# Performance work log

Measured on AMD Instinct MI355X. Metric: run time of the kernel, lower is better.

The kernel has to match this reference:

```python
import jax, jax.numpy as jnp
import numpy as np

K = 3      # kernel_size
PAD = 1    # padding


def _unfold(x, k, pad):
    # torch.nn.functional.unfold, stride=1, dilation=1.
    # Returns (B, C*k*k, L) with channel-major, then kernel-row, kernel-col ordering.
    B, C, H, W = x.shape
    xp = jnp.pad(x, ((0, 0), (0, 0), (pad, pad), (pad, pad)))
    Ho = H + 2 * pad - k + 1
    Wo = W + 2 * pad - k + 1
    cols = jnp.stack([xp[:, :, i:i + Ho, j:j + Wo]
                      for i in range(k) for j in range(k)], axis=2)  # (B,C,k*k,Ho,Wo)
    return cols.reshape(B, C * k * k, Ho * Wo)


def _fold_nonoverlap(pcols, C, k, pad, out_size):
    # torch.nn.functional.fold with kernel_size=k, stride=k (non-overlapping tiles),
    # padding=pad, output_size=(out_size, out_size).
    B = pcols.shape[0]
    bh = (out_size + 2 * pad - k) // k + 1  # blocks per spatial dim
    t = pcols.reshape(B, C, k, k, bh, bh)
    t = t.transpose(0, 1, 4, 2, 5, 3).reshape(B, C, bh * k, bh * k)  # tiled canvas
    # canvas position = tile position - pad; crop window [pad, pad+out_size)
    t = jnp.pad(t, ((0, 0), (0, 0), (0, pad), (0, pad)))
    return t[:, :, pad:pad + out_size, pad:pad + out_size]


def _cdist(a, b):
    # torch.cdist (p=2): (N,P) x (M,P) -> (N,M)
    a2 = jnp.sum(a * a, axis=1, keepdims=True)
    b2 = jnp.sum(b * b, axis=1)
    d2 = a2 + b2[None, :] - 2.0 * (a @ b.T)
    return jnp.sqrt(jnp.maximum(d2, 1e-12))


def setup_inputs() -> dict:
    key = jax.random.key(0)
    k1, k2, k3, k4 = jax.random.split(key, 4)
    B, Cin, H = 32, 64, 56
    Cout, num_centers = 128, 256
    P = Cin * K * K  # 576
    return {
        "x": jax.random.normal(k1, (B, Cin, H, H), dtype=jnp.float32),
        "weight": jax.random.normal(k2, (Cout, Cin, K, K), dtype=jnp.float32) * 0.05,
        "bias": jax.random.normal(k3, (Cout,), dtype=jnp.float32) * 0.05,
        "cluster_centers": jax.random.uniform(k4, (num_centers, P), dtype=jnp.float32),
        "temp": jnp.float32(1.0),
    }


def reference(x, weight, bias, cluster_centers, temp):
    B, Cin, H, W = x.shape
    patch_size = Cin * K * K

    this_patch = _unfold(x, K, PAD)                          # (B, C*K*K, L), L = H*W
    L = this_patch.shape[2]
    flat_patches = this_patch.transpose(0, 2, 1).reshape(-1, patch_size)  # (B*L, P)

    distances = _cdist(flat_patches, cluster_centers)        # (B*L, M)
    soft_assignments = jax.nn.softmax(-distances * temp, axis=1)
    transformed = soft_assignments @ cluster_centers         # (B*L, P)
    final_patches = (temp * transformed + flat_patches) / (temp + 1.0)

    # Faithful to torch: view_as is a raw reshape, NOT a transpose back.
    final_patches = final_patches.reshape(B, Cin * K * K, L)

    new_size = W * K
    x_refold = _fold_nonoverlap(final_patches, Cin, K, PAD, new_size)  # (B,Cin,HK,WK)

    out = jax.lax.conv_general_dilated(
        x_refold, weight,
        window_strides=(K, K),
        padding=((PAD, PAD), (PAD, PAD)),
        dimension_numbers=("NCHW", "OIHW", "NCHW"),
    )
    return out + bias[None, :, None, None]
```

## Files before the change

kernel.cpp:

```cpp
#include <hip/hip_runtime.h>
#include <hip/hip_bf16.h>

#define B_    32
#define CIN   64
#define HW    56
#define COUT  128
#define M_    256
#define P_    576
#define L_    3136
#define N_    100352

typedef __hip_bfloat16 bf16;
typedef unsigned short u16;
typedef __attribute__((ext_vector_type(8))) short bf16x8;
typedef __attribute__((ext_vector_type(8))) unsigned short u16x8;
typedef __attribute__((ext_vector_type(4))) float f32x4;

__device__ __forceinline__ float bits2f(u16 u){ return __uint_as_float(((unsigned)u) << 16); }
__device__ __forceinline__ u16 f2bf(float f){
  bf16 h = __float2bfloat16(f);
  return *(u16*)&h;
}

__global__ __launch_bounds__(256) void k0_prep(const float* __restrict__ C,
                                               const float* __restrict__ W,
                                               u16* __restrict__ CbP, u16* __restrict__ CtP,
                                               float* __restrict__ b2v, u16* __restrict__ WbP){
  __shared__ float red[4];
  const int t = threadIdx.x;
  const int bid = blockIdx.x;
  if (bid < M_){
    const int m = bid;
    float s = 0.f;
    for (int p = t; p < P_; p += 256){
      float vr = bits2f(f2bf(C[(size_t)m*P_ + p]));
      s += vr*vr;
    }
    #pragma unroll
    for (int off = 32; off >= 1; off >>= 1) s += __shfl_xor(s, off);
    if ((t & 63) == 0) red[t >> 6] = s;
    __syncthreads();
    if (t == 0) b2v[m] = red[0] + red[1] + red[2] + red[3];
  } else if (bid < M_ + 72){
    const int u = (bid - M_)*256 + t;
    const int f = u >> 6, lane = u & 63;
    const int g = lane >> 4, lr = lane & 15;
    const int k = f % 18, fj = f / 18;
    const int j = fj & 3, wvq = fj >> 2;
    const int m = wvq*64 + j*16 + lr;
    const int idx = k*4 + g;
    const int o = idx & 7, rr = idx >> 3;
    u16x8 o8;
    #pragma unroll
    for (int c = 0; c < 8; ++c) o8[c] = f2bf(C[(size_t)m*P_ + (o*8 + c)*9 + rr]);
    *(u16x8*)&CbP[(size_t)u*8] = o8;
  } else if (bid < M_ + 144){
    const int u = (bid - M_ - 72)*256 + t;
    const int f = u >> 6, lane = u & 63;
    const int g = lane >> 4, lr = lane & 15;
    const int mc = f & 7, fj = f >> 3;
    const int j = fj % 9, q = fj / 9;
    const int p = q*144 + j*16 + lr;
    const int m = mc*32 + g*8;
    u16x8 o8;
    #pragma unroll
    for (int c = 0; c < 8; ++c) o8[c] = f2bf(C[(size_t)(m + c)*P_ + p]);
    *(u16x8*)&CtP[(size_t)u*8] = o8;
  } else {
    const int u = (bid - M_ - 144)*256 + t;
    const int f = u >> 6, lane = u & 63;
    const int g = lane >> 4, lr = lane & 15;
    const int k = f % 18, fi = f / 18;
    const int i = fi & 3, wn = fi >> 2;
    const int co = wn*64 + i*16 + lr;
    const int q = k*32 + g*8;
    u16x8 o8;
    #pragma unroll
    for (int c = 0; c < 8; ++c) o8[c] = f2bf(W[(size_t)co*P_ + q + c]);
    *(u16x8*)&WbP[(size_t)u*8] = o8;
  }
}

__global__ __launch_bounds__(512, 4) void k123(const float* __restrict__ x,
    const u16* __restrict__ CbP, const u16* __restrict__ CtP,
    const float* __restrict__ b2v, const float* __restrict__ temp_p,
    u16* __restrict__ F){
  __shared__ __align__(16) char lds[76288];
  u16*   xt2 = (u16*)lds;
  char*  Bz  = lds + 36864;
  u16*   Sl  = (u16*)Bz;
  u16*   Fl  = (u16*)Bz;
  float* a2l = (float*)(lds + 74752);
  float* red = (float*)(lds + 75264);

  const int t = threadIdx.x;
  const int lane = t & 63;
  const int wv = t >> 6;
  const int ih = wv >> 2;
  const int mq = wv & 3;
  const int g  = lane >> 4;
  const int lr = lane & 15;
  const int blk_raw = blockIdx.x;
  const int blk = (blk_raw & 7) * 196 + (blk_raw >> 3);
  const int n0 = blk * 64;
  const int b  = n0 / L_;
  const int l0 = n0 - b * L_;
  const int h0 = l0 / 56;
  const float temp = *temp_p;

  const float* xb = x + (size_t)b * CIN * L_;
  {
    const int wc = t & 63;
    const int ix = wc - 1;
    #pragma unroll 4
    for (int iter = 0; iter < 32; ++iter){
      const int cw = (t >> 6) + iter*8;
      const int c  = cw & 63;
      const int ry = cw >> 6;
      const int iy = h0 - 1 + ry;
      float v = 0.f;
      if ((unsigned)iy < 56u && (unsigned)ix < 56u)
        v = xb[(size_t)c*L_ + iy*56 + ix];
      const int spat = ry*64 + wc;
      xt2[spat*72 + (((c>>3) + 2*spat) & 7)*8 + (c & 7)] = f2bf(v);
    }
  }
  __syncthreads();

  {
    const int l_  = l0 + mq*16 + lr;
    const int hwB = (l_/56 - h0)*64 + (l_ - (l_/56)*56);
    float s2 = 0.f;
    #pragma unroll
    for (int z = 0; z < 9; ++z){
      const int uu = (ih*9 + z)*4 + g;
      const int rr = uu >> 3, o = uu & 7;
      const int di = (rr >= 3) + (rr >= 6);
      const int spat = hwB + di*64 + (rr - di*3);
      u16x8 v8 = *(const u16x8*)&xt2[spat*72 + ((o + 2*spat) & 7)*8];
      #pragma unroll
      for (int c = 0; c < 8; ++c){
        const float vr = bits2f(v8[c]);
        s2 = fmaf(vr, vr, s2);
      }
    }
    s2 += __shfl_xor(s2, 16);
    s2 += __shfl_xor(s2, 32);
    if (g == 0) a2l[ih*64 + mq*16 + lr] = s2;
  }
  __syncthreads();

  int hw2[2];
  #pragma unroll
  for (int i = 0; i < 2; ++i){
    const int li = l0 + ih*32 + i*16 + lr;
    const int hi = li / 56;
    hw2[i] = (hi - h0)*64 + (li - hi*56);
  }

  f32x4 acc[2][4];
  #pragma unroll
  for (int i = 0; i < 2; ++i)
    #pragma unroll
    for (int j = 0; j < 4; ++j) acc[i][j] = (f32x4){0.f,0.f,0.f,0.f};

  bf16x8 bbc[4], bbn[4];
  #pragma unroll
  for (int j = 0; j < 4; ++j)
    bbc[j] = *(const bf16x8*)(CbP + (((size_t)(mq*4 + j)*18 + 0)*64 + lane)*8);

  #pragma unroll
  for (int kk = 0; kk < 18; ++kk){
    const int idx = kk*4 + g;
    const int rr = idx >> 3, o = idx & 7;
    const int di = (rr >= 3) + (rr >= 6);
    const int doff = di*64 + (rr - di*3);
    bf16x8 af[2];
    #pragma unroll
    for (int i = 0; i < 2; ++i){
      const int spat = hw2[i] + doff;
      af[i] = *(const bf16x8*)&xt2[spat*72 + ((o + 2*spat) & 7)*8];
    }
    if (kk + 1 < 18){
      #pragma unroll
      for (int j = 0; j < 4; ++j)
        bbn[j] = *(const bf16x8*)(CbP + (((size_t)(mq*4 + j)*18 + (kk+1))*64 + lane)*8);
    }
    #pragma unroll
    for (int i = 0; i < 2; ++i)
      #pragma unroll
      for (int j = 0; j < 4; ++j)
        acc[i][j] = __builtin_amdgcn_mfma_f32_16x16x32_bf16(af[i], bbc[j], acc[i][j], 0, 0, 0);
    if (kk + 1 < 18){
      #pragma unroll
      for (int j = 0; j < 4; ++j) bbc[j] = bbn[j];
    }
  }

  float a2r[2][4], b2r[4];
  #pragma unroll
  for (int i = 0; i < 2; ++i)
    #pragma unroll
    for (int r = 0; r < 4; ++r){
      const int row = ih*32 + i*16 + g*4 + r;
      a2r[i][r] = a2l[row] + a2l[64 + row];
    }
  #pragma unroll
  for (int j = 0; j < 4; ++j) b2r[j] = b2v[mq*64 + j*16 + lr];

  float rmax[2][4];
  #pragma unroll
  for (int i = 0; i < 2; ++i)
    #pragma unroll
    for (int r = 0; r < 4; ++r) rmax[i][r] = -3.4e38f;

  #pragma unroll
  for (int i = 0; i < 2; ++i)
    #pragma unroll
    for (int j = 0; j < 4; ++j)
      #pragma unroll
      for (int r = 0; r < 4; ++r){
        float d2 = fmaxf(a2r[i][r] + b2r[j] - 2.f*acc[i][j][r], 1e-12f);
        float lg = -temp * sqrtf(d2);
        acc[i][j][r] = lg;
        rmax[i][r] = fmaxf(rmax[i][r], lg);
      }
  #pragma unroll
  for (int i = 0; i < 2; ++i)
    #pragma unroll
    for (int r = 0; r < 4; ++r){
      float v = rmax[i][r];
      v = fmaxf(v, __shfl_xor(v, 1));
      v = fmaxf(v, __shfl_xor(v, 2));
      v = fmaxf(v, __shfl_xor(v, 4));
      v = fmaxf(v, __shfl_xor(v, 8));
      rmax[i][r] = v;
    }
  __syncthreads();
  if (lr == 0){
    #pragma unroll
    for (int i = 0; i < 2; ++i)
      #pragma unroll
      for (int r = 0; r < 4; ++r)
        red[mq*64 + ih*32 + i*16 + g*4 + r] = rmax[i][r];
  }
  __syncthreads();
  #pragma unroll
  for (int i = 0; i < 2; ++i)
    #pragma unroll
    for (int r = 0; r < 4; ++r){
      const int row = ih*32 + i*16 + g*4 + r;
      rmax[i][r] = fmaxf(fmaxf(red[row], red[64+row]), fmaxf(red[128+row], red[192+row]));
    }
  float rsum[2][4];
  #pragma unroll
  for (int i = 0; i < 2; ++i)
    #pragma unroll
    for (int r = 0; r < 4; ++r) rsum[i][r] = 0.f;
  #pragma unroll
  for (int i = 0; i < 2; ++i)
    #pragma unroll
    for (int j = 0; j < 4; ++j)
      #pragma unroll
      for (int r = 0; r < 4; ++r){
        float pe = __expf(acc[i][j][r] - rmax[i][r]);
        acc[i][j][r] = pe;
        rsum[i][r] += pe;
      }
  #pragma unroll
  for (int i = 0; i < 2; ++i)
    #pragma unroll
    for (int r = 0; r < 4; ++r){
      float v = rsum[i][r];
      v += __shfl_xor(v, 1);
      v += __shfl_xor(v, 2);
      v += __shfl_xor(v, 4);
      v += __shfl_xor(v, 8);
      rsum[i][r] = v;
    }
  __syncthreads();
  if (lr == 0){
    #pragma unroll
    for (int i = 0; i < 2; ++i)
      #pragma unroll
      for (int r = 0; r < 4; ++r)
        red[mq*64 + ih*32 + i*16 + g*4 + r] = rsum[i][r];
  }
  __syncthreads();
  #pragma unroll
  for (int i = 0; i < 2; ++i)
    #pragma unroll
    for (int r = 0; r < 4; ++r){
      const int row = ih*32 + i*16 + g*4 + r;
      const float invr = 1.f / (red[row] + red[64+row] + red[128+row] + red[192+row]);
      #pragma unroll
      for (int j = 0; j < 4; ++j)
        Sl[(size_t)row*264 + mq*64 + j*16 + lr] = f2bf(acc[i][j][r] * invr);
    }
  __syncthreads();

  f32x4 acc2[2][9];
  #pragma unroll
  for (int i = 0; i < 2; ++i)
    #pragma unroll
    for (int j = 0; j < 9; ++j) acc2[i][j] = (f32x4){0.f,0.f,0.f,0.f};

  for (int mc = 0; mc < 8; ++mc){
    bf16x8 af2[2], bb2[9];
    #pragma unroll
    for (int i = 0; i < 2; ++i)
      af2[i] = *(const bf16x8*)&Sl[(size_t)(ih*32 + i*16 + lr)*264 + mc*32 + g*8];
    #pragma unroll
    for (int j = 0; j < 9; ++j)
      bb2[j] = *(const bf16x8*)(CtP + (((size_t)(mq*9 + j)*8 + mc)*64 + lane)*8);
    #pragma unroll
    for (int j = 0; j < 9; ++j)
      #pragma unroll
      for (int i = 0; i < 2; ++i)
        acc2[i][j] = __builtin_amdgcn_mfma_f32_16x16x32_bf16(af2[i], bb2[j], acc2[i][j], 0, 0, 0);
  }

  const float inv = 1.f / (temp + 1.f);
  const float tscale = temp * inv;
  #pragma unroll
  for (int hh = 0; hh < 2; ++hh){
    __syncthreads();
    if ((mq >> 1) == hh){
      const int pbase = (mq & 1) * 144;
      #pragma unroll
      for (int i = 0; i < 2; ++i)
        #pragma unroll
        for (int j = 0; j < 9; ++j)
          #pragma unroll
          for (int r = 0; r < 4; ++r)
            Fl[(ih*32 + i*16 + g*4 + r)*296 + pbase + j*16 + lr] = f2bf(acc2[i][j][r] * tscale);
    }
    __syncthreads();
    for (int v = t; v < 2304; v += 512){
      const int row = v / 36, col = (v - row*36) * 8;
      u16x8 tv = *(const u16x8*)&Fl[row*296 + col];
      const int p0 = hh*288 + col;
      int ch2 = p0 / 9;
      int rr2 = p0 - ch2*9;
      const int l2 = l0 + row;
      const int h2 = l2 / 56;
      const int hb2 = (h2 - h0)*64 + (l2 - h2*56);
      u16x8 o;
      #pragma unroll
      for (int c2 = 0; c2 < 8; ++c2){
        const int di2 = (rr2 >= 3) + (rr2 >= 6);
        const int spat = hb2 + di2*64 + (rr2 - di2*3);
        const u16 av_ = xt2[spat*72 + (((ch2>>3) + 2*spat) & 7)*8 + (ch2 & 7)];
        o[c2] = f2bf(bits2f(tv[c2]) + bits2f(av_) * inv);
        const bool w9 = (rr2 == 8);
        rr2 = w9 ? 0 : rr2 + 1;
        ch2 += w9 ? 1 : 0;
      }
      *(u16x8*)(F + (size_t)(n0 + row)*P_ + hh*288 + col) = o;
    }
  }
}

__global__ __launch_bounds__(256) void k4_conv(const u16* __restrict__ F,
    const u16* __restrict__ WbP, const float* __restrict__ bias,
    float* __restrict__ out){
  __shared__ short Fl[128*40];
  const int t = threadIdx.x;
  const int lane = t & 63;
  const int w = t >> 6;
  const int wn = w >> 1;
  const int ws = w & 1;
  const int g  = lane >> 4;
  const int lr = lane & 15;
  const int b  = blockIdx.y;
  const int s0 = blockIdx.x * 128;
  const u16* Fb = F + (size_t)b * ((size_t)P_ * L_);

  f32x4 acc[4][4];
  #pragma unroll
  for (int i = 0; i < 4; ++i)
    #pragma unroll
    for (int j = 0; j < 4; ++j) acc[i][j] = (f32x4){0.f,0.f,0.f,0.f};

  for (int step = 0; step < 18; ++step){
    const int q0 = step * 32;
    __syncthreads();
    #pragma unroll
    for (int e = 0; e < 2; ++e){
      const int c = t + e*256;
      const int ql = c & 31, sch = c >> 5;
      const int q  = q0 + ql;
      const int sbase = s0 + sch*8;
      const int scl = (sbase < L_ - 8) ? sbase : (L_ - 8);
      u16x8 v = *(const u16x8*)(Fb + (size_t)q*L_ + scl);
      const int q3 = q/3;
      const bool kx0 = (q - q3*3) == 0;
      const bool ky0 = (q3 % 3) == 0;
      const int r0 = sbase % 56;
      #pragma unroll
      for (int u = 0; u < 8; ++u){
        const bool m0 = ky0 && (sbase + u) < 56;
        const bool m1 = kx0 && ((r0 + u) == 0 || (r0 + u) == 56);
        Fl[(sch*8 + u)*40 + ql] = (m0 || m1) ? (short)0 : (short)v[u];
      }
    }
    __syncthreads();
    bf16x8 af[4], bb[4];
    #pragma unroll
    for (int i = 0; i < 4; ++i)
      af[i] = *(const bf16x8*)(WbP + (((size_t)(wn*4 + i)*18 + step)*64 + lane)*8);
    #pragma unroll
    for (int j = 0; j < 4; ++j)
      bb[j] = *(const bf16x8*)&Fl[(ws*64 + j*16 + lr)*40 + g*8];
    #pragma unroll
    for (int i = 0; i < 4; ++i)
      #pragma unroll
      for (int j = 0; j < 4; ++j)
        acc[i][j] = __builtin_amdgcn_mfma_f32_16x16x32_bf16(af[i], bb[j], acc[i][j], 0, 0, 0);
  }

  #pragma unroll
  for (int i = 0; i < 4; ++i)
    #pragma unroll
    for (int r = 0; r < 4; ++r){
      const int co = wn*64 + i*16 + g*4 + r;
      const float bv = bias[co];
      #pragma unroll
      for (int j = 0; j < 4; ++j){
        const int s = s0 + ws*64 + j*16 + lr;
        if (s < L_) out[((size_t)b*COUT + co)*L_ + s] = acc[i][j][r] + bv;
      }
    }
}

extern "C" void kernel_launch(void* const* d_in, const int* in_sizes, int n_in,
                              void* d_out, int out_size, void* d_ws, size_t ws_size,
                              hipStream_t stream){
  const float* x      = (const float*)d_in[0];
  const float* weight = (const float*)d_in[1];
  const float* bias   = (const float*)d_in[2];
  const float* cc     = (const float*)d_in[3];
  const float* temp_p = (const float*)d_in[4];
  float* out = (float*)d_out;

  char* ws = (char*)d_ws;
  u16*   F   = (u16*)(ws);
  float* b2v = (float*)(ws + 115605504);
  u16*   CbP = (u16*)(ws + 115606528);
  u16*   CtP = (u16*)(ws + 115901440);
  u16*   WbP = (u16*)(ws + 116196352);

  k0_prep <<<436,          256, 0, stream>>>(cc, weight, CbP, CtP, b2v, WbP);
  k123    <<<N_/64,        512, 0, stream>>>(x, CbP, CtP, b2v, temp_p, F);
  k4_conv <<<dim3(25, B_), 256, 0, stream>>>(F, WbP, bias, out);
}
```

Before: 238.7 us.

## Double-buffer conv LDS tile and prefetch next global loads in registers

The conv kernel now uses two LDS buffers and register-prefetches the global F loads two steps ahead. This overlaps global memory latency and LDS stores with the MFMA work, and removes one barrier per step. In exchange it doubles LDS use per block and raises register pressure, which may lower occupancy.

New measurement: 214.4 us. 1.11x faster.

```diff
diff --git a/kernel.cpp b/kernel.cpp
--- a/kernel.cpp
+++ b/kernel.cpp
@@ -364,7 +364,7 @@
 __global__ __launch_bounds__(256) void k4_conv(const u16* __restrict__ F,
     const u16* __restrict__ WbP, const float* __restrict__ bias,
     float* __restrict__ out){
-  __shared__ short Fl[128*40];
+  __shared__ short Fl[2][128*40];
   const int t = threadIdx.x;
   const int lane = t & 63;
   const int w = t >> 6;
@@ -376,47 +376,79 @@
   const int s0 = blockIdx.x * 128;
   const u16* Fb = F + (size_t)b * ((size_t)P_ * L_);
 
+  const int ql  = t & 31;
+  const int sch = t >> 5;
+  const int sb0 = s0 + sch*8;
+  const int sb1 = s0 + (sch + 8)*8;
+  const int sc0 = (sb0 < L_ - 8) ? sb0 : (L_ - 8);
+  const int sc1 = (sb1 < L_ - 8) ? sb1 : (L_ - 8);
+  const int r00 = sb0 % 56;
+  const int r01 = sb1 % 56;
+
   f32x4 acc[4][4];
   #pragma unroll
   for (int i = 0; i < 4; ++i)
     #pragma unroll
     for (int j = 0; j < 4; ++j) acc[i][j] = (f32x4){0.f,0.f,0.f,0.f};
 
+  u16x8 vv0, vv1;
+  {
+    vv0 = *(const u16x8*)(Fb + (size_t)(0*32 + ql)*L_ + sc0);
+    vv1 = *(const u16x8*)(Fb + (size_t)(0*32 + ql)*L_ + sc1);
+    const int q = ql;
+    const int q3 = q/3;
+    const bool kx0 = (q - q3*3) == 0;
+    const bool ky0 = (q3 % 3) == 0;
+    #pragma unroll
+    for (int u = 0; u < 8; ++u){
+      const bool m0a = ky0 && (sb0 + u) < 56;
+      const bool m1a = kx0 && ((r00 + u) == 0 || (r00 + u) == 56);
+      Fl[0][(sch*8 + u)*40 + ql] = (m0a || m1a) ? (short)0 : (short)vv0[u];
+      const bool m0b = ky0 && (sb1 + u) < 56;
+      const bool m1b = kx0 && ((r01 + u) == 0 || (r01 + u) == 56);
+      Fl[0][((sch+8)*8 + u)*40 + ql] = (m0b || m1b) ? (short)0 : (short)vv1[u];
+    }
+    vv0 = *(const u16x8*)(Fb + (size_t)(1*32 + ql)*L_ + sc0);
+    vv1 = *(const u16x8*)(Fb + (size_t)(1*32 + ql)*L_ + sc1);
+  }
+  __syncthreads();
+
   for (int step = 0; step < 18; ++step){
-    const int q0 = step * 32;
-    __syncthreads();
-    #pragma unroll
-    for (int e = 0; e < 2; ++e){
-      const int c = t + e*256;
-      const int ql = c & 31, sch = c >> 5;
-      const int q  = q0 + ql;
-      const int sbase = s0 + sch*8;
-      const int scl = (sbase < L_ - 8) ? sbase : (L_ - 8);
-      u16x8 v = *(const u16x8*)(Fb + (size_t)q*L_ + scl);
+    const short* cur = Fl[step & 1];
+    bf16x8 af[4], bb[4];
+    #pragma unroll
+    for (int i = 0; i < 4; ++i)
+      af[i] = *(const bf16x8*)(WbP + (((size_t)(wn*4 + i)*18 + step)*64 + lane)*8);
+    #pragma unroll
+    for (int j = 0; j < 4; ++j)
+      bb[j] = *(const bf16x8*)&cur[(ws*64 + j*16 + lr)*40 + g*8];
+    #pragma unroll
+    for (int i = 0; i < 4; ++i)
+      #pragma unroll
+      for (int j = 0; j < 4; ++j)
+        acc[i][j] = __builtin_amdgcn_mfma_f32_16x16x32_bf16(af[i], bb[j], acc[i][j], 0, 0, 0);
+
+    if (step + 1 < 18){
+      short* nxt = Fl[(step + 1) & 1];
+      const int q = (step + 1)*32 + ql;
       const int q3 = q/3;
       const bool kx0 = (q - q3*3) == 0;
       const bool ky0 = (q3 % 3) == 0;
-      const int r0 = sbase % 56;
       #pragma unroll
       for (int u = 0; u < 8; ++u){
-        const bool m0 = ky0 && (sbase + u) < 56;
-        const bool m1 = kx0 && ((r0 + u) == 0 || (r0 + u) == 56);
-        Fl[(sch*8 + u)*40 + ql] = (m0 || m1) ? (short)0 : (short)v[u];
+        const bool m0a = ky0 && (sb0 + u) < 56;
+        const bool m1a = kx0 && ((r00 + u) == 0 || (r00 + u) == 56);
+        nxt[(sch*8 + u)*40 + ql] = (m0a || m1a) ? (short)0 : (short)vv0[u];
+        const bool m0b = ky0 && (sb1 + u) < 56;
+        const bool m1b = kx0 && ((r01 + u) == 0 || (r01 + u) == 56);
+        nxt[((sch+8)*8 + u)*40 + ql] = (m0b || m1b) ? (short)0 : (short)vv1[u];
+      }
+      if (step + 2 < 18){
+        vv0 = *(const u16x8*)(Fb + (size_t)((step+2)*32 + ql)*L_ + sc0);
+        vv1 = *(const u16x8*)(Fb + (size_t)((step+2)*32 + ql)*L_ + sc1);
       }
     }
     __syncthreads();
-    bf16x8 af[4], bb[4];
-    #pragma unroll
-    for (int i = 0; i < 4; ++i)
-      af[i] = *(const bf16x8*)(WbP + (((size_t)(wn*4 + i)*18 + step)*64 + lane)*8);
-    #pragma unroll
-    for (int j = 0; j < 4; ++j)
-      bb[j] = *(const bf16x8*)&Fl[(ws*64 + j*16 + lr)*40 + g*8];
-    #pragma unroll
-    for (int i = 0; i < 4; ++i)
-      #pragma unroll
-      for (int j = 0; j < 4; ++j)
-        acc[i][j] = __builtin_amdgcn_mfma_f32_16x16x32_bf16(af[i], bb[j], acc[i][j], 0, 0, 0);
   }
 
   #pragma unroll
```
